# Kernel optimization log

Hardware: AMD Instinct MI355X
Metric: run time of the kernel (lower is better)

The kernel has to match this reference:

```python
import jax, jax.numpy as jnp
import numpy as np

HEAD_SIZE = 128
NUM_EMBED = 1024
BLOCK_SIZE = 2048


def setup_inputs() -> dict:
    key = jax.random.key(0)
    kx, kk, kq, kv = jax.random.split(key, 4)
    x = jax.random.normal(kx, (4, BLOCK_SIZE, NUM_EMBED), dtype=jnp.float32)
    s = 1.0 / np.sqrt(NUM_EMBED)
    Wk = jax.random.normal(kk, (NUM_EMBED, HEAD_SIZE), dtype=jnp.float32) * s
    Wq = jax.random.normal(kq, (NUM_EMBED, HEAD_SIZE), dtype=jnp.float32) * s
    Wv = jax.random.normal(kv, (NUM_EMBED, HEAD_SIZE), dtype=jnp.float32) * s
    return {"x": x, "Wk": Wk, "Wq": Wq, "Wv": Wv}


def reference(x, Wk, Wq, Wv):
    # x: [B, T, C]; W*: [C, H]
    B, T, C = x.shape
    k = x @ Wk          # [B, T, H]
    q = x @ Wq          # [B, T, H]
    v = x @ Wv          # [B, T, H]
    scale = k.shape[-1] ** -0.5
    wei = jnp.einsum('bth,bsh->bts', q, k) * scale  # [B, T, T]
    causal = jnp.tril(jnp.ones((T, T), dtype=bool))
    wei = jnp.where(causal, wei, -jnp.inf)
    wei = jax.nn.softmax(wei, axis=-1)
    out = jnp.einsum('bts,bsh->bth', wei, v)        # [B, T, H]
    return out
```

## Files before the change

kernel.cpp:

```cpp
#include <hip/hip_runtime.h>
#include <hip/hip_bf16.h>
#include <math.h>

#define B_ 4
#define T_ 2048
#define C_ 1024
#define H_ 128
#define SCALE 0.088388347648318447f

typedef unsigned short u16;
typedef __bf16 bf16x8 __attribute__((ext_vector_type(8)));
typedef __bf16 bf16x4 __attribute__((ext_vector_type(4)));
typedef float  f32x4  __attribute__((ext_vector_type(4)));
typedef u16    u16x8  __attribute__((ext_vector_type(8)));
typedef u16    u16x4  __attribute__((ext_vector_type(4)));

__device__ __forceinline__ u16 f2bf(float f) {
    __hip_bfloat16 h = __float2bfloat16(f);
    return __builtin_bit_cast(u16, h);
}

__device__ __forceinline__ void load_lds16(const void* g, void* l) {
    __builtin_amdgcn_global_load_lds(
        (const __attribute__((address_space(1))) unsigned int*)g,
        (__attribute__((address_space(3))) unsigned int*)l, 16, 0, 0);
}

__global__ __launch_bounds__(256) void convert_x(const float* __restrict__ x,
                                                 u16* __restrict__ xb) {
    const size_t i = ((size_t)blockIdx.x * 256 + threadIdx.x) * 8;
    const float4 a = *(const float4*)&x[i];
    const float4 b = *(const float4*)&x[i + 4];
    u16x8 r;
    r[0] = f2bf(a.x); r[1] = f2bf(a.y); r[2] = f2bf(a.z); r[3] = f2bf(a.w);
    r[4] = f2bf(b.x); r[5] = f2bf(b.y); r[6] = f2bf(b.z); r[7] = f2bf(b.w);
    *(u16x8*)&xb[i] = r;
}

__global__ __launch_bounds__(256) void convert_w(const float* __restrict__ Wq,
                                                 const float* __restrict__ Wk,
                                                 const float* __restrict__ Wv,
                                                 u16* __restrict__ wbT) {
    const int id = blockIdx.x * 256 + threadIdx.x;
    const int s = id >> 17;
    const int r = id & 131071;
    const int k = r >> 7, n = r & 127;
    const float* W = (s == 0) ? Wq : (s == 1) ? Wk : Wv;
    float v = W[k * 128 + n];
    if (s == 0) v *= SCALE;
    wbT[(s << 17) + (n << 10) + k] = f2bf(v);
}

__global__ __launch_bounds__(256) void gemm_qkv(
    const u16* __restrict__ xb, const u16* __restrict__ wbT,
    u16* __restrict__ qb, u16* __restrict__ kb, u16* __restrict__ vT)
{
    __shared__ u16 xs[4096];
    __shared__ u16 ws[8192];

    const int tid = threadIdx.x;
    const int w = tid >> 6, lane = tid & 63, lg = lane >> 4, lr = lane & 15;
    const int wm = w >> 1, wn = w & 1;
    const int s = blockIdx.y;
    const int m0 = blockIdx.x * 64;
    const u16* wsrc = wbT + (s << 17);

    f32x4 acc[2][4] = {};

    for (int k0 = 0; k0 < C_; k0 += 64) {
        __syncthreads();
#pragma unroll
        for (int i = 0; i < 2; ++i) {
            const unsigned o = (unsigned)(w * 2 + i) * 1024u + (unsigned)lane * 16u;
            const unsigned o2 = o ^ (((o >> 7) & 7u) << 4);
            const unsigned row = o2 >> 7, col = (o2 & 127u) >> 1;
            load_lds16(xb + (size_t)(m0 + row) * C_ + k0 + col, &xs[(w * 2 + i) * 512]);
        }
#pragma unroll
        for (int i = 0; i < 4; ++i) {
            const unsigned o = (unsigned)(w * 4 + i) * 1024u + (unsigned)lane * 16u;
            const unsigned o2 = o ^ (((o >> 7) & 7u) << 4);
            const unsigned row = o2 >> 7, col = (o2 & 127u) >> 1;
            load_lds16(wsrc + (size_t)row * C_ + k0 + col, &ws[(w * 4 + i) * 512]);
        }
        __syncthreads();

#pragma unroll
        for (int kc = 0; kc < 2; ++kc) {
            bf16x8 af[2], bfr[4];
#pragma unroll
            for (int mi = 0; mi < 2; ++mi) {
                const int row = wm * 32 + mi * 16 + lr;
                const unsigned byte = (unsigned)(kc * 64 + lg * 16) ^ (((unsigned)row & 7u) << 4);
                af[mi] = *(const bf16x8*)((const char*)xs + row * 128 + byte);
            }
#pragma unroll
            for (int ni = 0; ni < 4; ++ni) {
                const int n = wn * 64 + ni * 16 + lr;
                const unsigned byte = (unsigned)(kc * 64 + lg * 16) ^ (((unsigned)n & 7u) << 4);
                bfr[ni] = *(const bf16x8*)((const char*)ws + n * 128 + byte);
            }
#pragma unroll
            for (int mi = 0; mi < 2; ++mi)
#pragma unroll
                for (int ni = 0; ni < 4; ++ni)
                    acc[mi][ni] = __builtin_amdgcn_mfma_f32_16x16x32_bf16(
                        af[mi], bfr[ni], acc[mi][ni], 0, 0, 0);
        }
    }

    if (s < 2) {
        u16* dst = (s == 0) ? qb : kb;
#pragma unroll
        for (int mi = 0; mi < 2; ++mi)
#pragma unroll
            for (int ni = 0; ni < 4; ++ni) {
                const int trow = m0 + wm * 32 + mi * 16 + lg * 4;
                const int col = wn * 64 + ni * 16 + lr;
#pragma unroll
                for (int r = 0; r < 4; ++r)
                    dst[(size_t)(trow + r) * H_ + col] = f2bf(acc[mi][ni][r]);
            }
    } else {
#pragma unroll
        for (int mi = 0; mi < 2; ++mi)
#pragma unroll
            for (int ni = 0; ni < 4; ++ni) {
                const int trow = m0 + wm * 32 + mi * 16 + lg * 4;
                const int bb = trow >> 11, t = trow & 2047;
                const int d = wn * 64 + ni * 16 + lr;
                u16x4 pk;
                pk[0] = f2bf(acc[mi][ni][0]); pk[1] = f2bf(acc[mi][ni][1]);
                pk[2] = f2bf(acc[mi][ni][2]); pk[3] = f2bf(acc[mi][ni][3]);
                *(u16x4*)&vT[((size_t)bb * 128 + d) * 2048 + t] = pk;
            }
    }
}

__global__ __launch_bounds__(128) void attn_split(
    const u16* __restrict__ qb, const u16* __restrict__ kb,
    const u16* __restrict__ vT, float* __restrict__ po, float* __restrict__ ml)
{
    __shared__ u16 ks[4096];
    __shared__ u16 vs[128 * 36];

    const int jt = blockIdx.x, sp = blockIdx.y, b = blockIdx.z;
    if (sp * 16 > jt) return;
    const int kt0 = sp * 16;
    const int kt_end = min(kt0 + 16, jt + 1);

    const int tid = threadIdx.x;
    const int w = tid >> 6, lane = tid & 63, lg = lane >> 4, lr = lane & 15;
    const int qrow_base = jt * 32 + w * 16;

    const u16* qp = qb + ((size_t)(b << 11) + qrow_base + lr) * H_;
    bf16x8 qf[4];
#pragma unroll
    for (int kc = 0; kc < 4; ++kc)
        qf[kc] = *(const bf16x8*)&qp[kc * 32 + lg * 8];

    f32x4 o[8] = {};
    float m_run = -INFINITY, l_run = 0.f;

    for (int kt = kt0; kt < kt_end; ++kt) {
        __syncthreads();
        const u16* kbase = kb + ((size_t)(b << 11) + kt * 32) * H_;
#pragma unroll
        for (int i = 0; i < 4; ++i) {
            const unsigned o_ = (unsigned)(w * 4 + i) * 1024u + (unsigned)lane * 16u;
            const unsigned o2 = o_ ^ (((o_ >> 8) & 7u) << 4);
            const unsigned row = o2 >> 8, colb = o2 & 255u;
            load_lds16((const char*)kbase + row * 256 + colb, &ks[(w * 4 + i) * 512]);
        }
        const u16* vbase = vT + (size_t)b * 128 * 2048 + (size_t)kt * 32;
#pragma unroll
        for (int i = 0; i < 4; ++i) {
            const int idx = i * 128 + tid;
            const int d = idx >> 2, c = idx & 3;
            const u16x8 tmp = *(const u16x8*)&vbase[(size_t)d * 2048 + c * 8];
            *(u16x8*)((char*)vs + d * 72 + c * 16) = tmp;
        }
        __syncthreads();

        f32x4 s0 = {0.f, 0.f, 0.f, 0.f}, s1 = {0.f, 0.f, 0.f, 0.f};
        const unsigned swz = ((unsigned)lr & 7u) << 4;
#pragma unroll
        for (int kc = 0; kc < 4; ++kc) {
            const unsigned byte = ((unsigned)(kc * 64 + lg * 16)) ^ swz;
            const bf16x8 kf0 = *(const bf16x8*)((const char*)ks + lr * 256 + byte);
            const bf16x8 kf1 = *(const bf16x8*)((const char*)ks + lr * 256 + 4096 + byte);
            s0 = __builtin_amdgcn_mfma_f32_16x16x32_bf16(kf0, qf[kc], s0, 0, 0, 0);
            s1 = __builtin_amdgcn_mfma_f32_16x16x32_bf16(kf1, qf[kc], s1, 0, 0, 0);
        }

        if (kt == jt) {
            const int qq = w * 16 + lr;
#pragma unroll
            for (int r = 0; r < 4; ++r) {
                if (lg * 4 + r > qq)      s0[r] = -INFINITY;
                if (16 + lg * 4 + r > qq) s1[r] = -INFINITY;
            }
        }

        float mt = fmaxf(fmaxf(fmaxf(s0[0], s0[1]), fmaxf(s0[2], s0[3])),
                         fmaxf(fmaxf(s1[0], s1[1]), fmaxf(s1[2], s1[3])));
        mt = fmaxf(mt, __shfl_xor(mt, 16));
        mt = fmaxf(mt, __shfl_xor(mt, 32));
        const float mn = fmaxf(m_run, mt);
        const float p0 = __expf(s0[0] - mn), p1 = __expf(s0[1] - mn);
        const float p2 = __expf(s0[2] - mn), p3 = __expf(s0[3] - mn);
        const float p4 = __expf(s1[0] - mn), p5 = __expf(s1[1] - mn);
        const float p6 = __expf(s1[2] - mn), p7 = __expf(s1[3] - mn);
        float sum = ((p0 + p1) + (p2 + p3)) + ((p4 + p5) + (p6 + p7));
        sum += __shfl_xor(sum, 16);
        sum += __shfl_xor(sum, 32);
        const float f = __expf(m_run - mn);
        l_run = l_run * f + sum;
        m_run = mn;

        const float fb0 = __shfl(f, lg * 4 + 0);
        const float fb1 = __shfl(f, lg * 4 + 1);
        const float fb2 = __shfl(f, lg * 4 + 2);
        const float fb3 = __shfl(f, lg * 4 + 3);
#pragma unroll
        for (int ni = 0; ni < 8; ++ni) {
            o[ni][0] *= fb0; o[ni][1] *= fb1; o[ni][2] *= fb2; o[ni][3] *= fb3;
        }

        bf16x8 pa;
        pa[0] = (__bf16)p0; pa[1] = (__bf16)p1; pa[2] = (__bf16)p2; pa[3] = (__bf16)p3;
        pa[4] = (__bf16)p4; pa[5] = (__bf16)p5; pa[6] = (__bf16)p6; pa[7] = (__bf16)p7;

#pragma unroll
        for (int ni = 0; ni < 8; ++ni) {
            const int n = ni * 16 + lr;
            const char* vrow = (const char*)vs + n * 72;
            const bf16x4 vlo = *(const bf16x4*)(vrow + lg * 8);
            const bf16x4 vhi = *(const bf16x4*)(vrow + 32 + lg * 8);
            bf16x8 vf;
            vf[0] = vlo[0]; vf[1] = vlo[1]; vf[2] = vlo[2]; vf[3] = vlo[3];
            vf[4] = vhi[0]; vf[5] = vhi[1]; vf[6] = vhi[2]; vf[7] = vhi[3];
            o[ni] = __builtin_amdgcn_mfma_f32_16x16x32_bf16(pa, vf, o[ni], 0, 0, 0);
        }
    }

    const int g = jt >> 4, rr = jt & 15;
    const int slot = (g + 1) * (8 * g + rr) + sp;
    float* pob = po + (size_t)(b * 160 + slot) * 32 * 128;
#pragma unroll
    for (int ni = 0; ni < 8; ++ni) {
        const int col = ni * 16 + lr;
#pragma unroll
        for (int rj = 0; rj < 4; ++rj)
            pob[(w * 16 + lg * 4 + rj) * 128 + col] = o[ni][rj];
    }
    if (lg == 0) {
        float* mlb = ml + (size_t)(b * 160 + slot) * 64;
        mlb[w * 16 + lr] = m_run;
        mlb[32 + w * 16 + lr] = l_run;
    }
}

__global__ __launch_bounds__(256) void attn_combine(
    const float* __restrict__ po, const float* __restrict__ ml,
    float* __restrict__ out)
{
    const int rid = (blockIdx.x << 3) + (threadIdx.x >> 5);
    const int b = blockIdx.y;
    const int d4 = (threadIdx.x & 31) * 4;
    const int jt = rid >> 5, row = rid & 31;
    const int g = jt >> 4, rr = jt & 15;
    const int slot0 = (g + 1) * (8 * g + rr);
    const int c = g + 1;

    float M = -INFINITY;
#pragma unroll
    for (int si = 0; si < 4; ++si)
        if (si < c) M = fmaxf(M, ml[(size_t)(b * 160 + slot0 + si) * 64 + row]);

    float L = 0.f;
    float a0 = 0.f, a1 = 0.f, a2 = 0.f, a3 = 0.f;
#pragma unroll
    for (int si = 0; si < 4; ++si) {
        if (si < c) {
            const float* mlb = ml + (size_t)(b * 160 + slot0 + si) * 64;
            const float wgt = __expf(mlb[row] - M);
            L += wgt * mlb[32 + row];
            const float4 t = *(const float4*)&po[((size_t)(b * 160 + slot0 + si) * 32 + row) * 128 + d4];
            a0 = fmaf(wgt, t.x, a0); a1 = fmaf(wgt, t.y, a1);
            a2 = fmaf(wgt, t.z, a2); a3 = fmaf(wgt, t.w, a3);
        }
    }
    const float inv = 1.f / L;
    *(float4*)&out[((size_t)(b << 11) + rid) * H_ + d4] =
        make_float4(a0 * inv, a1 * inv, a2 * inv, a3 * inv);
}

extern "C" void kernel_launch(void* const* d_in, const int* in_sizes, int n_in,
                              void* d_out, int out_size, void* d_ws, size_t ws_size,
                              hipStream_t stream) {
    const float* x  = (const float*)d_in[0];
    const float* Wk = (const float*)d_in[1];
    const float* Wq = (const float*)d_in[2];
    const float* Wv = (const float*)d_in[3];
    float* out = (float*)d_out;

    u16* xb  = (u16*)d_ws;
    u16* wbT = xb + 8388608;
    u16* qb  = wbT + 393216;
    u16* kb  = qb + 1048576;
    u16* vT  = kb + 1048576;

    float* po = (float*)d_ws;
    float* ml = (float*)((char*)d_ws + 16777216);

    convert_x<<<4096, 256, 0, stream>>>(x, xb);
    convert_w<<<1536, 256, 0, stream>>>(Wq, Wk, Wv, wbT);
    gemm_qkv<<<dim3(128, 3), 256, 0, stream>>>(xb, wbT, qb, kb, vT);
    attn_split<<<dim3(64, 4, 4), 128, 0, stream>>>(qb, kb, vT, po, ml);
    attn_combine<<<dim3(256, 4), 256, 0, stream>>>(po, ml, out);
}
```

Before: 65.97 us.

## Fuse x conversion into QKV GEMM, double-buffer attention tiles, finer KV split

The separate fp32-to-bf16 pass over x is removed. The QKV GEMM now loads fp32 x directly, converts it in registers and writes it swizzled to LDS, which avoids writing and re-reading a bf16 copy of x. The attention kernel double-buffers its K and V tiles: it prefetches the next tile while computing on the current one, and each iteration needs one barrier instead of two. The KV split is also halved to 8 tiles per block, with twice as many splits and a matching slot layout in the combine kernel. This adds parallelism but also more partial-output traffic and merge work, and the GEMM must now read x at fp32 width from global memory three times, once per output projection.

```diff
diff --git a/kernel.cpp b/kernel.cpp
--- a/kernel.cpp
+++ b/kernel.cpp
@@ -15,6 +15,13 @@
 typedef u16    u16x8  __attribute__((ext_vector_type(8)));
 typedef u16    u16x4  __attribute__((ext_vector_type(4)));
 
+#define PO_OFF  0u
+#define ML_OFF  18874368u
+#define WBT_OFF 19169280u
+#define QB_OFF  19955712u
+#define KB_OFF  22052864u
+#define VT_OFF  24150016u
+
 __device__ __forceinline__ u16 f2bf(float f) {
     __hip_bfloat16 h = __float2bfloat16(f);
     return __builtin_bit_cast(u16, h);
@@ -24,17 +31,6 @@
     __builtin_amdgcn_global_load_lds(
         (const __attribute__((address_space(1))) unsigned int*)g,
         (__attribute__((address_space(3))) unsigned int*)l, 16, 0, 0);
-}
-
-__global__ __launch_bounds__(256) void convert_x(const float* __restrict__ x,
-                                                 u16* __restrict__ xb) {
-    const size_t i = ((size_t)blockIdx.x * 256 + threadIdx.x) * 8;
-    const float4 a = *(const float4*)&x[i];
-    const float4 b = *(const float4*)&x[i + 4];
-    u16x8 r;
-    r[0] = f2bf(a.x); r[1] = f2bf(a.y); r[2] = f2bf(a.z); r[3] = f2bf(a.w);
-    r[4] = f2bf(b.x); r[5] = f2bf(b.y); r[6] = f2bf(b.z); r[7] = f2bf(b.w);
-    *(u16x8*)&xb[i] = r;
 }
 
 __global__ __launch_bounds__(256) void convert_w(const float* __restrict__ Wq,
@@ -52,7 +48,7 @@
 }
 
 __global__ __launch_bounds__(256) void gemm_qkv(
-    const u16* __restrict__ xb, const u16* __restrict__ wbT,
+    const float* __restrict__ x, const u16* __restrict__ wbT,
     u16* __restrict__ qb, u16* __restrict__ kb, u16* __restrict__ vT)
 {
     __shared__ u16 xs[4096];
@@ -65,23 +61,33 @@
     const int m0 = blockIdx.x * 64;
     const u16* wsrc = wbT + (s << 17);
 
+    const int xrow = tid >> 2;
+    const int xseg = tid & 3;
+
     f32x4 acc[2][4] = {};
 
     for (int k0 = 0; k0 < C_; k0 += 64) {
+        const float4* xp = (const float4*)&x[(size_t)(m0 + xrow) * C_ + k0 + xseg * 16];
+        const float4 f0 = xp[0], f1 = xp[1], f2 = xp[2], f3 = xp[3];
+
         __syncthreads();
-#pragma unroll
-        for (int i = 0; i < 2; ++i) {
-            const unsigned o = (unsigned)(w * 2 + i) * 1024u + (unsigned)lane * 16u;
-            const unsigned o2 = o ^ (((o >> 7) & 7u) << 4);
-            const unsigned row = o2 >> 7, col = (o2 & 127u) >> 1;
-            load_lds16(xb + (size_t)(m0 + row) * C_ + k0 + col, &xs[(w * 2 + i) * 512]);
-        }
 #pragma unroll
         for (int i = 0; i < 4; ++i) {
             const unsigned o = (unsigned)(w * 4 + i) * 1024u + (unsigned)lane * 16u;
             const unsigned o2 = o ^ (((o >> 7) & 7u) << 4);
             const unsigned row = o2 >> 7, col = (o2 & 127u) >> 1;
             load_lds16(wsrc + (size_t)row * C_ + k0 + col, &ws[(w * 4 + i) * 512]);
+        }
+        {
+            u16x8 lo, hi;
+            lo[0] = f2bf(f0.x); lo[1] = f2bf(f0.y); lo[2] = f2bf(f0.z); lo[3] = f2bf(f0.w);
+            lo[4] = f2bf(f1.x); lo[5] = f2bf(f1.y); lo[6] = f2bf(f1.z); lo[7] = f2bf(f1.w);
+            hi[0] = f2bf(f2.x); hi[1] = f2bf(f2.y); hi[2] = f2bf(f2.z); hi[3] = f2bf(f2.w);
+            hi[4] = f2bf(f3.x); hi[5] = f2bf(f3.y); hi[6] = f2bf(f3.z); hi[7] = f2bf(f3.w);
+            const unsigned sw = ((unsigned)xrow & 7u) << 4;
+            char* rb = (char*)xs + xrow * 128;
+            *(u16x8*)(rb + (((unsigned)xseg * 32 + 0) ^ sw)) = lo;
+            *(u16x8*)(rb + (((unsigned)xseg * 32 + 16) ^ sw)) = hi;
         }
         __syncthreads();
 
@@ -141,54 +147,82 @@
     const u16* __restrict__ qb, const u16* __restrict__ kb,
     const u16* __restrict__ vT, float* __restrict__ po, float* __restrict__ ml)
 {
-    __shared__ u16 ks[4096];
-    __shared__ u16 vs[128 * 36];
+    __shared__ u16 ks[2][4096];
+    __shared__ u16 vs[2][128 * 36];
 
     const int jt = blockIdx.x, sp = blockIdx.y, b = blockIdx.z;
-    if (sp * 16 > jt) return;
-    const int kt0 = sp * 16;
-    const int kt_end = min(kt0 + 16, jt + 1);
+    if (sp * 8 > jt) return;
+    const int kt0 = sp * 8;
+    const int kt_end = min(kt0 + 8, jt + 1);
 
     const int tid = threadIdx.x;
     const int w = tid >> 6, lane = tid & 63, lg = lane >> 4, lr = lane & 15;
     const int qrow_base = jt * 32 + w * 16;
 
+    const u16* kbB = kb + ((size_t)(b << 11)) * H_;
+    const u16* vbB = vT + (size_t)b * 128 * 2048;
+
+    unsigned krow[4], kcolb[4];
+#pragma unroll
+    for (int i = 0; i < 4; ++i) {
+        const unsigned o_ = (unsigned)(w * 4 + i) * 1024u + (unsigned)lane * 16u;
+        const unsigned o2 = o_ ^ (((o_ >> 8) & 7u) << 4);
+        krow[i] = o2 >> 8; kcolb[i] = o2 & 255u;
+    }
+    int vd[4], vc[4];
+#pragma unroll
+    for (int i = 0; i < 4; ++i) {
+        const int idx = i * 128 + tid;
+        vd[i] = idx >> 2; vc[i] = idx & 3;
+    }
+
     const u16* qp = qb + ((size_t)(b << 11) + qrow_base + lr) * H_;
     bf16x8 qf[4];
 #pragma unroll
     for (int kc = 0; kc < 4; ++kc)
         qf[kc] = *(const bf16x8*)&qp[kc * 32 + lg * 8];
 
+    u16x8 vr[4];
+    {
+        const u16* kbase = kbB + (size_t)kt0 * 32 * H_;
+#pragma unroll
+        for (int i = 0; i < 4; ++i)
+            load_lds16((const char*)kbase + krow[i] * 256 + kcolb[i], &ks[0][(w * 4 + i) * 512]);
+        const u16* vbase = vbB + (size_t)kt0 * 32;
+#pragma unroll
+        for (int i = 0; i < 4; ++i)
+            vr[i] = *(const u16x8*)&vbase[(size_t)vd[i] * 2048 + vc[i] * 8];
+#pragma unroll
+        for (int i = 0; i < 4; ++i)
+            *(u16x8*)((char*)vs[0] + vd[i] * 72 + vc[i] * 16) = vr[i];
+    }
+    __syncthreads();
+
     f32x4 o[8] = {};
     float m_run = -INFINITY, l_run = 0.f;
+    int cur = 0;
 
     for (int kt = kt0; kt < kt_end; ++kt) {
-        __syncthreads();
-        const u16* kbase = kb + ((size_t)(b << 11) + kt * 32) * H_;
-#pragma unroll
-        for (int i = 0; i < 4; ++i) {
-            const unsigned o_ = (unsigned)(w * 4 + i) * 1024u + (unsigned)lane * 16u;
-            const unsigned o2 = o_ ^ (((o_ >> 8) & 7u) << 4);
-            const unsigned row = o2 >> 8, colb = o2 & 255u;
-            load_lds16((const char*)kbase + row * 256 + colb, &ks[(w * 4 + i) * 512]);
-        }
-        const u16* vbase = vT + (size_t)b * 128 * 2048 + (size_t)kt * 32;
-#pragma unroll
-        for (int i = 0; i < 4; ++i) {
-            const int idx = i * 128 + tid;
-            const int d = idx >> 2, c = idx & 3;
-            const u16x8 tmp = *(const u16x8*)&vbase[(size_t)d * 2048 + c * 8];
-            *(u16x8*)((char*)vs + d * 72 + c * 16) = tmp;
-        }
-        __syncthreads();
+        const bool pf = (kt + 1 < kt_end);
+        if (pf) {
+            const u16* kbase = kbB + (size_t)(kt + 1) * 32 * H_;
+#pragma unroll
+            for (int i = 0; i < 4; ++i)
+                load_lds16((const char*)kbase + krow[i] * 256 + kcolb[i],
+                           &ks[cur ^ 1][(w * 4 + i) * 512]);
+            const u16* vbase = vbB + (size_t)(kt + 1) * 32;
+#pragma unroll
+            for (int i = 0; i < 4; ++i)
+                vr[i] = *(const u16x8*)&vbase[(size_t)vd[i] * 2048 + vc[i] * 8];
+        }
 
         f32x4 s0 = {0.f, 0.f, 0.f, 0.f}, s1 = {0.f, 0.f, 0.f, 0.f};
         const unsigned swz = ((unsigned)lr & 7u) << 4;
 #pragma unroll
         for (int kc = 0; kc < 4; ++kc) {
             const unsigned byte = ((unsigned)(kc * 64 + lg * 16)) ^ swz;
-            const bf16x8 kf0 = *(const bf16x8*)((const char*)ks + lr * 256 + byte);
-            const bf16x8 kf1 = *(const bf16x8*)((const char*)ks + lr * 256 + 4096 + byte);
+            const bf16x8 kf0 = *(const bf16x8*)((const char*)ks[cur] + lr * 256 + byte);
+            const bf16x8 kf1 = *(const bf16x8*)((const char*)ks[cur] + lr * 256 + 4096 + byte);
             s0 = __builtin_amdgcn_mfma_f32_16x16x32_bf16(kf0, qf[kc], s0, 0, 0, 0);
             s1 = __builtin_amdgcn_mfma_f32_16x16x32_bf16(kf1, qf[kc], s1, 0, 0, 0);
         }
@@ -234,7 +268,7 @@
 #pragma unroll
         for (int ni = 0; ni < 8; ++ni) {
             const int n = ni * 16 + lr;
-            const char* vrow = (const char*)vs + n * 72;
+            const char* vrow = (const char*)vs[cur] + n * 72;
             const bf16x4 vlo = *(const bf16x4*)(vrow + lg * 8);
             const bf16x4 vhi = *(const bf16x4*)(vrow + 32 + lg * 8);
             bf16x8 vf;
@@ -242,11 +276,19 @@
             vf[4] = vhi[0]; vf[5] = vhi[1]; vf[6] = vhi[2]; vf[7] = vhi[3];
             o[ni] = __builtin_amdgcn_mfma_f32_16x16x32_bf16(pa, vf, o[ni], 0, 0, 0);
         }
-    }
-
-    const int g = jt >> 4, rr = jt & 15;
-    const int slot = (g + 1) * (8 * g + rr) + sp;
-    float* pob = po + (size_t)(b * 160 + slot) * 32 * 128;
+
+        if (pf) {
+#pragma unroll
+            for (int i = 0; i < 4; ++i)
+                *(u16x8*)((char*)vs[cur ^ 1] + vd[i] * 72 + vc[i] * 16) = vr[i];
+        }
+        __syncthreads();
+        cur ^= 1;
+    }
+
+    const int g = jt >> 3, rr = jt & 7;
+    const int slot = (g + 1) * (4 * g + rr) + sp;
+    float* pob = po + (size_t)(b * 288 + slot) * 32 * 128;
 #pragma unroll
     for (int ni = 0; ni < 8; ++ni) {
         const int col = ni * 16 + lr;
@@ -255,7 +297,7 @@
             pob[(w * 16 + lg * 4 + rj) * 128 + col] = o[ni][rj];
     }
     if (lg == 0) {
-        float* mlb = ml + (size_t)(b * 160 + slot) * 64;
+        float* mlb = ml + (size_t)(b * 288 + slot) * 64;
         mlb[w * 16 + lr] = m_run;
         mlb[32 + w * 16 + lr] = l_run;
     }
@@ -269,24 +311,24 @@
     const int b = blockIdx.y;
     const int d4 = (threadIdx.x & 31) * 4;
     const int jt = rid >> 5, row = rid & 31;
-    const int g = jt >> 4, rr = jt & 15;
-    const int slot0 = (g + 1) * (8 * g + rr);
+    const int g = jt >> 3, rr = jt & 7;
+    const int slot0 = (g + 1) * (4 * g + rr);
     const int c = g + 1;
 
     float M = -INFINITY;
 #pragma unroll
-    for (int si = 0; si < 4; ++si)
-        if (si < c) M = fmaxf(M, ml[(size_t)(b * 160 + slot0 + si) * 64 + row]);
+    for (int si = 0; si < 8; ++si)
+        if (si < c) M = fmaxf(M, ml[(size_t)(b * 288 + slot0 + si) * 64 + row]);
 
     float L = 0.f;
     float a0 = 0.f, a1 = 0.f, a2 = 0.f, a3 = 0.f;
 #pragma unroll
-    for (int si = 0; si < 4; ++si) {
+    for (int si = 0; si < 8; ++si) {
         if (si < c) {
-            const float* mlb = ml + (size_t)(b * 160 + slot0 + si) * 64;
+            const float* mlb = ml + (size_t)(b * 288 + slot0 + si) * 64;
             const float wgt = __expf(mlb[row] - M);
             L += wgt * mlb[32 + row];
-            const float4 t = *(const float4*)&po[((size_t)(b * 160 + slot0 + si) * 32 + row) * 128 + d4];
+            const float4 t = *(const float4*)&po[((size_t)(b * 288 + slot0 + si) * 32 + row) * 128 + d4];
             a0 = fmaf(wgt, t.x, a0); a1 = fmaf(wgt, t.y, a1);
             a2 = fmaf(wgt, t.z, a2); a3 = fmaf(wgt, t.w, a3);
         }
@@ -305,18 +347,15 @@
     const float* Wv = (const float*)d_in[3];
     float* out = (float*)d_out;
 
-    u16* xb  = (u16*)d_ws;
-    u16* wbT = xb + 8388608;
-    u16* qb  = wbT + 393216;
-    u16* kb  = qb + 1048576;
-    u16* vT  = kb + 1048576;
-
-    float* po = (float*)d_ws;
-    float* ml = (float*)((char*)d_ws + 16777216);
-
-    convert_x<<<4096, 256, 0, stream>>>(x, xb);
+    float* po = (float*)((char*)d_ws + PO_OFF);
+    float* ml = (float*)((char*)d_ws + ML_OFF);
+    u16* wbT  = (u16*)((char*)d_ws + WBT_OFF);
+    u16* qb   = (u16*)((char*)d_ws + QB_OFF);
+    u16* kb   = (u16*)((char*)d_ws + KB_OFF);
+    u16* vT   = (u16*)((char*)d_ws + VT_OFF);
+
     convert_w<<<1536, 256, 0, stream>>>(Wq, Wk, Wv, wbT);
-    gemm_qkv<<<dim3(128, 3), 256, 0, stream>>>(xb, wbT, qb, kb, vT);
-    attn_split<<<dim3(64, 4, 4), 128, 0, stream>>>(qb, kb, vT, po, ml);
+    gemm_qkv<<<dim3(128, 3), 256, 0, stream>>>(x, wbT, qb, kb, vT);
+    attn_split<<<dim3(64, 8, 4), 128, 0, stream>>>(qb, kb, vT, po, ml);
     attn_combine<<<dim3(256, 4), 256, 0, stream>>>(po, ml, out);
 }
```

Measured after the change: 64.61 us. -2.1%, faster.
